# Performance work log

Hardware: AMD Instinct MI355X
Metric: run time of the kernel (lower is better)

## Reference

```python
import jax, jax.numpy as jnp
import numpy as np

KERNEL_MUL = 2.0
KERNEL_NUM = 5


def setup_inputs() -> dict:
    key = jax.random.key(0)
    k1, k2 = jax.random.split(key)
    source = jax.random.normal(k1, (4096, 512), dtype=jnp.float32)
    target = jax.random.normal(k2, (4096, 512), dtype=jnp.float32)
    return {"source": source, "target": target}


def reference(source, target):
    b = source.shape[0]
    total = jnp.concatenate([source, target], axis=0)  # [N, D]
    n = total.shape[0]
    # pairwise squared L2 via dot-product trick (same math as expand-subtract)
    sq = jnp.sum(total * total, axis=1)  # [N]
    L2 = sq[:, None] + sq[None, :] - 2.0 * (total @ total.T)  # [N, N]
    # bandwidth uses .data in torch -> constant w.r.t. grads
    bw = jax.lax.stop_gradient(jnp.sum(L2)) / (n * n - n)
    bw = bw / (KERNEL_MUL ** (KERNEL_NUM // 2))
    kernels = jnp.zeros_like(L2)
    for i in range(KERNEL_NUM):  # small fixed loop over bandwidths
        kernels = kernels + jnp.exp(-L2 / (bw * (KERNEL_MUL ** i)))
    XX = jnp.mean(kernels[:b, :b])
    YY = jnp.mean(kernels[b:, b:])
    XY = jnp.mean(kernels[:b, b:])
    YX = jnp.mean(kernels[b:, :b])
    return XX + YY - XY - YX
```

## Files before the change

kernel.cpp:

```cpp
#include <hip/hip_runtime.h>
#include <cstdint>
#include <cstddef>


#define D_DIM 512
#define B_ROWS 4096
#define N_ROWS 8192
#define NTILES 64
#define NBLK_MMD 2080
#define LDS_HALF 8192
#define LDS_BUF 16384

typedef __attribute__((ext_vector_type(4))) int i32x4;

__device__ inline float waveReduce(float v) {
    #pragma unroll
    for (int off = 32; off > 0; off >>= 1) v += __shfl_down(v, off, 64);
    return v;
}

__device__ inline int q8(float x) {
    int v = (int)rintf(x * 16.f);
    v = v > 127 ? 127 : v;
    v = v < -127 ? -127 : v;
    return v & 255;
}


__global__ __launch_bounds__(256) void k_rowstats(const float* __restrict__ src,
                                                  const float* __restrict__ tgt,
                                                  unsigned char* __restrict__ Tp,
                                                  float* __restrict__ sq) {
    int wave = threadIdx.x >> 6;
    int lane = threadIdx.x & 63;
    int row  = blockIdx.x * 4 + wave;
    const float* base = (row < B_ROWS) ? (src + (size_t)row * D_DIM)
                                       : (tgt + (size_t)(row - B_ROWS) * D_DIM);
    float4 a = ((const float4*)base)[lane * 2];
    float4 b = ((const float4*)base)[lane * 2 + 1];
    uint2 o;
    o.x = (unsigned)(q8(a.x) | (q8(a.y) << 8) | (q8(a.z) << 16) | (q8(a.w) << 24));
    o.y = (unsigned)(q8(b.x) | (q8(b.y) << 8) | (q8(b.z) << 16) | (q8(b.w) << 24));
    int rb = row >> 4, w = row & 15;
    int c  = lane >> 1, h = lane & 1;
    *(uint2*)(Tp + (((size_t)(rb * 32 + c)) << 8) + w * 16 + h * 8) = o;
    float s = a.x*a.x + a.y*a.y + a.z*a.z + a.w*a.w
            + b.x*b.x + b.y*b.y + b.z*b.z + b.w*b.w;
    s = waveReduce(s);
    if (lane == 0) sq[row] = s;
}

__global__ __launch_bounds__(256) void k_colsum(const unsigned int* __restrict__ Tu,
                                                int* __restrict__ partial) {
    int t   = threadIdx.x;
    int u   = t & 127;
    int c   = u >> 2, q = u & 3;
    int sub = t >> 7;
    int a0 = 0, a1 = 0, a2 = 0, a3 = 0;
    #pragma unroll 2
    for (int j = 0; j < 8; ++j) {
        int rb = blockIdx.x * 8 + j;
        #pragma unroll
        for (int wv = 0; wv < 8; ++wv) {
            int w = sub * 8 + wv;
            unsigned int v = Tu[(size_t)(rb * 32 + c) * 64 + w * 4 + q];
            a0 += (int)(signed char)(v);
            a1 += (int)(signed char)(v >> 8);
            a2 += (int)(signed char)(v >> 16);
            a3 += (int)(signed char)(v >> 24);
        }
    }
    int basep = (blockIdx.x * 2 + sub) * 512 + u * 4;
    partial[basep + 0] = a0;
    partial[basep + 1] = a1;
    partial[basep + 2] = a2;
    partial[basep + 3] = a3;
}

__global__ __launch_bounds__(512) void k_bw(const int* __restrict__ partial,
                                            const float* __restrict__ sq,
                                            float* __restrict__ c16out) {
    int t = threadIdx.x;
    int csum = 0;
    #pragma unroll 8
    for (int i = 0; i < 128; ++i) csum += partial[i * 512 + t];
    float cs = (float)csum * 0.0625f;
    float p = cs * cs;
    float ssq = 0.f;
    #pragma unroll
    for (int i = 0; i < 16; ++i) ssq += sq[t + i * 512];
    __shared__ float r8[8], q8s[8];
    float wp = waveReduce(p);
    float wq = waveReduce(ssq);
    if ((t & 63) == 0) { r8[t >> 6] = wp; q8s[t >> 6] = wq; }
    __syncthreads();
    if (t == 0) {
        double P = 0.0, Q = 0.0;
        #pragma unroll
        for (int i = 0; i < 8; ++i) { P += r8[i]; Q += q8s[i]; }
        double n = (double)N_ROWS;
        double sumL2 = 2.0 * n * Q - 2.0 * P;
        double bw = sumL2 / (n * n - n) / 4.0;
        c16out[0] = (float)(-1.4426950408889634 / (16.0 * bw));
    }
}

__global__ __launch_bounds__(256) void k_mmd(const unsigned char* __restrict__ Tp,
                                             const float* __restrict__ sq,
                                             const float* __restrict__ c16in,
                                             float* __restrict__ blockpart) {
    int bid = (int)blockIdx.x;
    bid = (bid & 7) * 260 + (bid >> 3);

    int rem = bid;
    int ti = 0, rowlen = NTILES;
    while (rem >= rowlen) { rem -= rowlen; rowlen--; ti++; }
    int tj = ti + rem;

    int tid  = threadIdx.x;
    int wave = tid >> 6;
    int lane = tid & 63;
    int waveM = (wave >> 1) * 64;
    int waveN = (wave & 1) * 64;
    int l15   = lane & 15;
    int quad  = lane >> 4;

    float c16 = c16in[0];
    float cgq = -2.f * c16 * (1.f / 256.f);

    int rbA0 = ti * 8;
    int rbB0 = tj * 8;

    __shared__ unsigned char lds[2 * LDS_BUF];

    i32x4 acc[4][4];
    #pragma unroll
    for (int mi = 0; mi < 4; ++mi)
        #pragma unroll
        for (int ni = 0; ni < 4; ++ni)
            acc[mi][ni] = (i32x4){0, 0, 0, 0};

    auto stage = [&](int buf, int kk) {
        unsigned char* lbase = lds + buf * LDS_BUF;
        #pragma unroll
        for (int s = 0; s < 2; ++s) {
            int rbl = wave * 2 + s;
            const unsigned char* gA =
                Tp + (((size_t)((rbA0 + rbl) * 32 + kk * 4)) << 8) + lane * 16;
            const unsigned char* gB =
                Tp + (((size_t)((rbB0 + rbl) * 32 + kk * 4)) << 8) + lane * 16;
            __builtin_amdgcn_global_load_lds(
                (const __attribute__((address_space(1))) void*)gA,
                (__attribute__((address_space(3))) void*)(lbase + rbl * 1024 + lane * 16),
                16, 0, 0);
            __builtin_amdgcn_global_load_lds(
                (const __attribute__((address_space(1))) void*)gB,
                (__attribute__((address_space(3))) void*)(lbase + LDS_HALF + rbl * 1024 + lane * 16),
                16, 0, 0);
        }
    };

    stage(0, 0);
    __syncthreads();

    int aoff = ((wave >> 1) * 4) * 1024 + quad * 256 + l15 * 16;
    int boff = ((wave & 1) * 4) * 1024 + quad * 256 + l15 * 16;

    int buf = 0;
    for (int kk = 0; kk < 8; ++kk) {
        if (kk < 7) stage(buf ^ 1, kk + 1);

        const unsigned char* bufA = lds + buf * LDS_BUF;
        const unsigned char* bufB = bufA + LDS_HALF;
        i32x4 af[4], bf[4];
        #pragma unroll
        for (int mi = 0; mi < 4; ++mi)
            af[mi] = *(const i32x4*)(bufA + aoff + mi * 1024);
        #pragma unroll
        for (int ni = 0; ni < 4; ++ni)
            bf[ni] = *(const i32x4*)(bufB + boff + ni * 1024);
        #pragma unroll
        for (int mi = 0; mi < 4; ++mi)
            #pragma unroll
            for (int ni = 0; ni < 4; ++ni)
                acc[mi][ni] = __builtin_amdgcn_mfma_i32_16x16x64_i8(
                    af[mi], bf[ni], acc[mi][ni], 0, 0, 0);

        __syncthreads();
        buf ^= 1;
    }

    const float* sqA = sq + ti * 128;
    const float* sqB = sq + tj * 128;
    float trow16[16];
    #pragma unroll
    for (int mi = 0; mi < 4; ++mi)
        #pragma unroll
        for (int r = 0; r < 4; ++r)
            trow16[mi * 4 + r] = sqA[waveM + mi * 16 + quad * 4 + r] * c16;
    float tcol16[4];
    #pragma unroll
    for (int ni = 0; ni < 4; ++ni)
        tcol16[ni] = sqB[waveN + ni * 16 + l15] * c16;

    bool dtile = (ti == tj);
    float psum = 0.f;
    #pragma unroll
    for (int mi = 0; mi < 4; ++mi) {
        #pragma unroll
        for (int ni = 0; ni < 4; ++ni) {
            #pragma unroll
            for (int r = 0; r < 4; ++r) {
                float g   = (float)acc[mi][ni][r];
                float t16 = __builtin_fmaf(g, cgq, trow16[mi * 4 + r]) + tcol16[ni];
                float e1  = __builtin_amdgcn_exp2f(t16);
                float e2  = e1 * e1;
                float e4  = e2 * e2;
                float e8  = e4 * e4;
                float e16 = e8 * e8;
                float ks5 = ((e1 + e2) + (e4 + e8)) + e16;
                int rl = waveM + mi * 16 + quad * 4 + r;
                int cl = waveN + ni * 16 + l15;
                psum += (dtile && rl == cl) ? 5.0f : ks5;
            }
        }
    }

    float* red = (float*)lds;
    float w = waveReduce(psum);
    if (lane == 0) red[wave] = w;
    __syncthreads();
    if (tid == 0) {
        float tot   = red[0] + red[1] + red[2] + red[3];
        float sign  = ((ti < 32) == (tj < 32)) ? 1.f : -1.f;
        float scale = (ti == tj) ? sign : 2.f * sign;
        blockpart[bid] = tot * scale;
    }
}

__global__ __launch_bounds__(256) void k_final(const float* __restrict__ bp,
                                               float* __restrict__ out) {
    int t = threadIdx.x;
    float s = 0.f;
    for (int i = t; i < NBLK_MMD; i += 256) s += bp[i];
    __shared__ float r4[4];
    float w = waveReduce(s);
    if ((t & 63) == 0) r4[t >> 6] = w;
    __syncthreads();
    if (t == 0)
        out[0] = (r4[0] + r4[1] + r4[2] + r4[3]) * (1.f / (4096.f * 4096.f));
}

extern "C" void kernel_launch(void* const* d_in, const int* in_sizes, int n_in,
                              void* d_out, int out_size, void* d_ws, size_t ws_size,
                              hipStream_t stream) {
    const float* src = (const float*)d_in[0];
    const float* tgt = (const float*)d_in[1];

    uint8_t* ws = (uint8_t*)d_ws;
    unsigned char* Tp = (unsigned char*)ws;
    size_t off = 4194304;
    float* sq      = (float*)(ws + off); off += 32768;
    int*   partial = (int*)  (ws + off); off += 128 * 512 * 4;
    float* bp      = (float*)(ws + off); off += 8320;
    float* c16     = (float*)(ws + off);

    k_rowstats<<<2048, 256, 0, stream>>>(src, tgt, Tp, sq);
    k_colsum  <<<64, 256, 0, stream>>>((const unsigned int*)Tp, partial);
    k_bw      <<<1, 512, 0, stream>>>(partial, sq, c16);
    k_mmd     <<<NBLK_MMD, 256, 0, stream>>>(Tp, sq, c16, bp);
    k_final   <<<1, 256, 0, stream>>>(bp, (float*)d_out);
}
```

Measured before the change: 109.2 us.

## Fuse bandwidth and final reduction into preceding kernels via last-block atomics

Merges the single-block bandwidth kernel into the column-sum kernel, and the final sum into the MMD kernel. In both cases the last block to finish, found with an atomic counter, does the reduction. Counters are reset in the row-stats kernel. This removes two kernel launches and their serialization gaps, and the epilogue branch is split so off-diagonal tiles skip the diagonal check. It adds atomics and thread fences, and puts a serial reduction tail on whichever block finishes last.

```diff
diff --git a/kernel.cpp b/kernel.cpp
--- a/kernel.cpp
+++ b/kernel.cpp
@@ -30,7 +30,12 @@
 __global__ __launch_bounds__(256) void k_rowstats(const float* __restrict__ src,
                                                   const float* __restrict__ tgt,
                                                   unsigned char* __restrict__ Tp,
-                                                  float* __restrict__ sq) {
+                                                  float* __restrict__ sq,
+                                                  unsigned int* __restrict__ cnt) {
+    if (blockIdx.x == 0 && threadIdx.x == 0) {
+        cnt[0] = 0u;
+        cnt[1] = 0u;
+    }
     int wave = threadIdx.x >> 6;
     int lane = threadIdx.x & 63;
     int row  = blockIdx.x * 4 + wave;
@@ -50,8 +55,11 @@
     if (lane == 0) sq[row] = s;
 }
 
-__global__ __launch_bounds__(256) void k_colsum(const unsigned int* __restrict__ Tu,
-                                                int* __restrict__ partial) {
+__global__ __launch_bounds__(256) void k_colbw(const unsigned int* __restrict__ Tu,
+                                               const float* __restrict__ sq,
+                                               int* __restrict__ partial,
+                                               float* __restrict__ c16out,
+                                               unsigned int* __restrict__ cnt) {
     int t   = threadIdx.x;
     int u   = t & 127;
     int c   = u >> 2, q = u & 3;
@@ -75,29 +83,39 @@
     partial[basep + 1] = a1;
     partial[basep + 2] = a2;
     partial[basep + 3] = a3;
-}
-
-__global__ __launch_bounds__(512) void k_bw(const int* __restrict__ partial,
-                                            const float* __restrict__ sq,
-                                            float* __restrict__ c16out) {
-    int t = threadIdx.x;
-    int csum = 0;
+
+    __shared__ bool isLast;
+    __syncthreads();
+    if (t == 0) {
+        __threadfence();
+        isLast = (atomicAdd(cnt, 1u) == 63u);
+    }
+    __syncthreads();
+    if (!isLast) return;
+    __threadfence();
+
+    float p = 0.f;
+    #pragma unroll
+    for (int cc = 0; cc < 2; ++cc) {
+        int col = t + cc * 256;
+        int csum = 0;
+        #pragma unroll 8
+        for (int i = 0; i < 128; ++i) csum += partial[i * 512 + col];
+        float cs = (float)csum * 0.0625f;
+        p += cs * cs;
+    }
+    float ssq = 0.f;
     #pragma unroll 8
-    for (int i = 0; i < 128; ++i) csum += partial[i * 512 + t];
-    float cs = (float)csum * 0.0625f;
-    float p = cs * cs;
-    float ssq = 0.f;
-    #pragma unroll
-    for (int i = 0; i < 16; ++i) ssq += sq[t + i * 512];
-    __shared__ float r8[8], q8s[8];
+    for (int i = 0; i < 32; ++i) ssq += sq[t + i * 256];
+    __shared__ float r4[4], q4[4];
     float wp = waveReduce(p);
     float wq = waveReduce(ssq);
-    if ((t & 63) == 0) { r8[t >> 6] = wp; q8s[t >> 6] = wq; }
+    if ((t & 63) == 0) { r4[t >> 6] = wp; q4[t >> 6] = wq; }
     __syncthreads();
     if (t == 0) {
         double P = 0.0, Q = 0.0;
         #pragma unroll
-        for (int i = 0; i < 8; ++i) { P += r8[i]; Q += q8s[i]; }
+        for (int i = 0; i < 4; ++i) { P += r4[i]; Q += q4[i]; }
         double n = (double)N_ROWS;
         double sumL2 = 2.0 * n * Q - 2.0 * P;
         double bw = sumL2 / (n * n - n) / 4.0;
@@ -108,9 +126,11 @@
 __global__ __launch_bounds__(256) void k_mmd(const unsigned char* __restrict__ Tp,
                                              const float* __restrict__ sq,
                                              const float* __restrict__ c16in,
-                                             float* __restrict__ blockpart) {
-    int bid = (int)blockIdx.x;
-    bid = (bid & 7) * 260 + (bid >> 3);
+                                             float* __restrict__ blockpart,
+                                             float* __restrict__ out,
+                                             unsigned int* __restrict__ cnt) {
+    int hwbid = (int)blockIdx.x;
+    int bid = (hwbid & 7) * 260 + (hwbid >> 3);
 
     int rem = bid;
     int ti = 0, rowlen = NTILES;
@@ -203,30 +223,50 @@
     for (int ni = 0; ni < 4; ++ni)
         tcol16[ni] = sqB[waveN + ni * 16 + l15] * c16;
 
-    bool dtile = (ti == tj);
     float psum = 0.f;
-    #pragma unroll
-    for (int mi = 0; mi < 4; ++mi) {
-        #pragma unroll
-        for (int ni = 0; ni < 4; ++ni) {
+    if (ti != tj) {
+        #pragma unroll
+        for (int mi = 0; mi < 4; ++mi) {
             #pragma unroll
-            for (int r = 0; r < 4; ++r) {
-                float g   = (float)acc[mi][ni][r];
-                float t16 = __builtin_fmaf(g, cgq, trow16[mi * 4 + r]) + tcol16[ni];
-                float e1  = __builtin_amdgcn_exp2f(t16);
-                float e2  = e1 * e1;
-                float e4  = e2 * e2;
-                float e8  = e4 * e4;
-                float e16 = e8 * e8;
-                float ks5 = ((e1 + e2) + (e4 + e8)) + e16;
-                int rl = waveM + mi * 16 + quad * 4 + r;
-                int cl = waveN + ni * 16 + l15;
-                psum += (dtile && rl == cl) ? 5.0f : ks5;
+            for (int ni = 0; ni < 4; ++ni) {
+                #pragma unroll
+                for (int r = 0; r < 4; ++r) {
+                    float g   = (float)acc[mi][ni][r];
+                    float t16 = __builtin_fmaf(g, cgq, trow16[mi * 4 + r]) + tcol16[ni];
+                    float e1  = __builtin_amdgcn_exp2f(t16);
+                    float e2  = e1 * e1;
+                    float e4  = e2 * e2;
+                    float e8  = e4 * e4;
+                    float e16 = e8 * e8;
+                    psum += ((e1 + e2) + (e4 + e8)) + e16;
+                }
             }
         }
+    } else {
+        #pragma unroll
+        for (int mi = 0; mi < 4; ++mi) {
+            #pragma unroll
+            for (int ni = 0; ni < 4; ++ni) {
+                #pragma unroll
+                for (int r = 0; r < 4; ++r) {
+                    float g   = (float)acc[mi][ni][r];
+                    float t16 = __builtin_fmaf(g, cgq, trow16[mi * 4 + r]) + tcol16[ni];
+                    float e1  = __builtin_amdgcn_exp2f(t16);
+                    float e2  = e1 * e1;
+                    float e4  = e2 * e2;
+                    float e8  = e4 * e4;
+                    float e16 = e8 * e8;
+                    float ks5 = ((e1 + e2) + (e4 + e8)) + e16;
+                    int rl = waveM + mi * 16 + quad * 4 + r;
+                    int cl = waveN + ni * 16 + l15;
+                    psum += (rl == cl) ? 5.0f : ks5;
+                }
+            }
+        }
     }
 
     float* red = (float*)lds;
+    __shared__ bool isLast;
     float w = waveReduce(psum);
     if (lane == 0) red[wave] = w;
     __syncthreads();
@@ -234,21 +274,21 @@
         float tot   = red[0] + red[1] + red[2] + red[3];
         float sign  = ((ti < 32) == (tj < 32)) ? 1.f : -1.f;
         float scale = (ti == tj) ? sign : 2.f * sign;
-        blockpart[bid] = tot * scale;
-    }
-}
-
-__global__ __launch_bounds__(256) void k_final(const float* __restrict__ bp,
-                                               float* __restrict__ out) {
-    int t = threadIdx.x;
+        blockpart[hwbid] = tot * scale;
+        __threadfence();
+        isLast = (atomicAdd(cnt, 1u) == NBLK_MMD - 1);
+    }
+    __syncthreads();
+    if (!isLast) return;
+    __threadfence();
+
     float s = 0.f;
-    for (int i = t; i < NBLK_MMD; i += 256) s += bp[i];
-    __shared__ float r4[4];
-    float w = waveReduce(s);
-    if ((t & 63) == 0) r4[t >> 6] = w;
-    __syncthreads();
-    if (t == 0)
-        out[0] = (r4[0] + r4[1] + r4[2] + r4[3]) * (1.f / (4096.f * 4096.f));
+    for (int i = tid; i < NBLK_MMD; i += 256) s += blockpart[i];
+    float ws = waveReduce(s);
+    if (lane == 0) red[wave] = ws;
+    __syncthreads();
+    if (tid == 0)
+        out[0] = (red[0] + red[1] + red[2] + red[3]) * (1.f / (4096.f * 4096.f));
 }
 
 extern "C" void kernel_launch(void* const* d_in, const int* in_sizes, int n_in,
@@ -263,11 +303,10 @@
     float* sq      = (float*)(ws + off); off += 32768;
     int*   partial = (int*)  (ws + off); off += 128 * 512 * 4;
     float* bp      = (float*)(ws + off); off += 8320;
-    float* c16     = (float*)(ws + off);
-
-    k_rowstats<<<2048, 256, 0, stream>>>(src, tgt, Tp, sq);
-    k_colsum  <<<64, 256, 0, stream>>>((const unsigned int*)Tp, partial);
-    k_bw      <<<1, 512, 0, stream>>>(partial, sq, c16);
-    k_mmd     <<<NBLK_MMD, 256, 0, stream>>>(Tp, sq, c16, bp);
-    k_final   <<<1, 256, 0, stream>>>(bp, (float*)d_out);
-}
+    float* c16     = (float*)(ws + off); off += 64;
+    unsigned int* cnt = (unsigned int*)(ws + off);
+
+    k_rowstats<<<2048, 256, 0, stream>>>(src, tgt, Tp, sq, cnt);
+    k_colbw   <<<64, 256, 0, stream>>>((const unsigned int*)Tp, sq, partial, c16, cnt);
+    k_mmd     <<<NBLK_MMD, 256, 0, stream>>>(Tp, sq, c16, bp, (float*)d_out, cnt + 1);
+}
```

Result: slower. 149.3 us (+36.7%).
